# Kernel tuning notes

Hardware: AMD Instinct MI355X
Metric: run time of the kernel (lower is better)

## Reference

```python
import jax, jax.numpy as jnp
import numpy as np

N = 10000
E = 160000
F_IN = 2000
HID = 128
NC = 5


def setup_inputs() -> dict:
    key = jax.random.key(0)
    ks = jax.random.split(key, 16)
    s = 0.05
    nrm = lambda k, shape: jax.random.normal(k, shape, jnp.float32) * s
    return {
        "x": jax.random.normal(ks[0], (N, F_IN), jnp.float32),
        "edge_index": jax.random.randint(ks[1], (2, E), 0, N),
        # GATConv 1: in=F_IN, out=HID, heads=6, concat=False
        "W_gat1": nrm(ks[2], (F_IN, 6 * HID)), "a_src1": nrm(ks[3], (6, HID)),
        "a_dst1": nrm(ks[4], (6, HID)), "b_gat1": jnp.zeros(HID, jnp.float32),
        # GCNConv 1
        "W_gcn1": nrm(ks[5], (HID, HID)), "b_gcn1": jnp.zeros(HID, jnp.float32),
        # GATConv 2: heads=4
        "W_gat2": nrm(ks[6], (HID, 4 * HID)), "a_src2": nrm(ks[7], (4, HID)),
        "a_dst2": nrm(ks[8], (4, HID)), "b_gat2": jnp.zeros(HID, jnp.float32),
        # GCNConv 2: out=HID//2
        "W_gcn2": nrm(ks[9], (HID, HID // 2)), "b_gcn2": jnp.zeros(HID // 2, jnp.float32),
        # skip projection / fusion
        "W_skip": nrm(ks[10], (F_IN, HID // 2)), "b_skip": jnp.zeros(HID // 2, jnp.float32),
        "W_fuse": nrm(ks[11], (HID + HID // 2, HID // 2)), "b_fuse": jnp.zeros(HID // 2, jnp.float32),
        # classifier MLP
        "W_c1": nrm(ks[12], (HID // 2, HID // 4)), "b_c1": jnp.zeros(HID // 4, jnp.float32),
        "W_c2": nrm(ks[13], (HID // 4, HID // 8)), "b_c2": jnp.zeros(HID // 8, jnp.float32),
        "W_c3": nrm(ks[14], (HID // 8, NC)), "b_c3": jnp.zeros(NC, jnp.float32),
        # LayerNorms
        "g1": jnp.ones(HID, jnp.float32), "be1": jnp.zeros(HID, jnp.float32),
        "g2": jnp.ones(HID, jnp.float32), "be2": jnp.zeros(HID, jnp.float32),
        "g3": jnp.ones(HID // 2, jnp.float32), "be3": jnp.zeros(HID // 2, jnp.float32),
    }


def layer_norm(x, g, b, eps=1e-5):
    mu = jnp.mean(x, axis=-1, keepdims=True)
    var = jnp.var(x, axis=-1, keepdims=True)
    return (x - mu) * jax.lax.rsqrt(var + eps) * g + b


def gat_conv(x, src, dst, W, a_src, a_dst, b, n):
    # PyG GATConv with concat=False (head-mean). Eval mode -> no attn dropout.
    H, C = a_src.shape
    h = (x @ W).reshape(-1, H, C)                      # [N,H,C]
    alpha = (h * a_src).sum(-1)[src] + (h * a_dst).sum(-1)[dst]  # [E,H]
    alpha = jax.nn.leaky_relu(alpha, 0.2)
    m = jax.ops.segment_max(alpha, dst, num_segments=n)
    e = jnp.exp(alpha - m[dst])
    w = e / jax.ops.segment_sum(e, dst, num_segments=n)[dst]     # segment softmax over incoming edges
    out = jax.ops.segment_sum(h[src] * w[:, :, None], dst, num_segments=n)  # [N,H,C]
    return out.mean(axis=1) + b


def gcn_conv(x, src, dst, W, b, n):
    deg = jax.ops.segment_sum(jnp.ones_like(dst, x.dtype), dst, num_segments=n)
    dinv = jnp.where(deg > 0, deg ** -0.5, 0.0)
    msg = (x @ W)[src] * (dinv[src] * dinv[dst])[:, None]
    return jax.ops.segment_sum(msg, dst, num_segments=n) + b


def reference(x, edge_index, W_gat1, a_src1, a_dst1, b_gat1, W_gcn1, b_gcn1,
              W_gat2, a_src2, a_dst2, b_gat2, W_gcn2, b_gcn2,
              W_skip, b_skip, W_fuse, b_fuse, W_c1, b_c1, W_c2, b_c2, W_c3, b_c3,
              g1, be1, g2, be2, g3, be3):
    n = x.shape[0]
    loop = jnp.arange(n, dtype=edge_index.dtype)
    src = jnp.concatenate([edge_index[0], loop])  # add_self_loops
    dst = jnp.concatenate([edge_index[1], loop])

    x1_gat = jax.nn.relu(layer_norm(gat_conv(x, src, dst, W_gat1, a_src1, a_dst1, b_gat1, n), g1, be1))
    x1_gcn = jax.nn.relu(gcn_conv(x1_gat, src, dst, W_gcn1, b_gcn1, n))
    x2_gat = jax.nn.relu(layer_norm(gat_conv(x1_gcn, src, dst, W_gat2, a_src2, a_dst2, b_gat2, n), g2, be2))
    x2_gcn = jax.nn.relu(gcn_conv(x2_gat, src, dst, W_gcn2, b_gcn2, n))

    skip = jax.nn.relu(x @ W_skip + b_skip)
    fused = jax.nn.relu(jnp.concatenate([x1_gcn, x2_gcn], axis=1) @ W_fuse + b_fuse)
    final = layer_norm(fused + skip, g3, be3)

    h = jax.nn.relu(final @ W_c1 + b_c1)
    h = jax.nn.relu(h @ W_c2 + b_c2)
    return h @ W_c3 + b_c3
```

## Files before the change

### kernel.cpp

```cpp
#include <hip/hip_runtime.h>
#include <cstdint>
#include <cstddef>

#define NN 10000
#define NE 160000
#define ET (NE + NN)
#define FIN 2000
#define MPAD 10112
#define KPAD 2048
#define NPAD 896

typedef __bf16 bf16x8 __attribute__((ext_vector_type(8)));
typedef __bf16 bf16x4 __attribute__((ext_vector_type(4)));
typedef float  f32x4  __attribute__((ext_vector_type(4)));

#define GLL(src, dst) __builtin_amdgcn_global_load_lds( \
    (const __attribute__((address_space(1))) void*)(src), \
    (__attribute__((address_space(3))) void*)(dst), 16, 0, 0)

__device__ __forceinline__ void edge_sd(const int* ei, int e, int& s, int& d) {
    if (e < NE) { s = ei[e]; d = ei[NE + e]; }
    else        { s = e - NE; d = e - NE; }
}

__global__ void scan_kernel(const int* deg, int* rowstart, float* dinv) {
    __shared__ int partial[256];
    const int T = 256;
    int chunk = (NN + T - 1) / T;
    int t = threadIdx.x;
    int begin = t * chunk;
    int end = begin + chunk; if (end > NN) end = NN;
    int s = 0;
    for (int i = begin; i < end && i >= begin; i++) s += deg[i];
    partial[t] = s;
    __syncthreads();
    if (t == 0) {
        int run = 0;
        for (int i = 0; i < T; i++) { int v = partial[i]; partial[i] = run; run += v; }
    }
    __syncthreads();
    int run = partial[t];
    for (int i = begin; i < end && i >= begin; i++) {
        rowstart[i] = run; run += deg[i];
        int dg = deg[i];
        dinv[i] = dg > 0 ? rsqrtf((float)dg) : 0.f;
    }
    if (end == NN && begin <= NN) rowstart[NN] = run;
}

__global__ void scatter_kernel(const int* ei, const int* rowstart, int* cursor,
                               int* csr_src) {
    int e = blockIdx.x * blockDim.x + threadIdx.x;
    if (e >= ET) return;
    int s, d; edge_sd(ei, e, s, d);
    int pos = atomicAdd(&cursor[d], 1);
    csr_src[rowstart[d] + pos] = s;
}

#define NBX (158 * 8)
#define NW1 (NPAD * KPAD / 8)
#define NWT (NW1 + 512 * 128 / 8)
#define NWT2 (NWT + 2048 + 1024)
#define WBLK ((NWT2 + 255) / 256)
#define EB 665
__global__ void conv_kernel(const float* __restrict__ x, __bf16* __restrict__ xb,
                            const float* __restrict__ Wg, const float* __restrict__ Ws,
                            const float* __restrict__ W2,
                            const float* __restrict__ Wg1, const float* __restrict__ Wg2,
                            __bf16* __restrict__ wt, __bf16* __restrict__ w2t,
                            __bf16* __restrict__ wgcn1s, __bf16* __restrict__ wgcn2s,
                            const int* __restrict__ ei, int* __restrict__ deg) {
    __shared__ __bf16 ls[16384];
    int bid = blockIdx.x;
    int tid = threadIdx.x;
    if (bid < NBX) {
        int rt = bid >> 3, kb = bid & 7;
        const int lane16 = tid & 15;
        const int ksl = lane16 >> 2;
        const int p0 = (lane16 & 3) * 2;
        const int rbase = tid >> 4;
        const int kg0 = kb * 256 + lane16 * 16;
        const int rsw_x = (p0 & 6) ^ ksl;
#pragma unroll
        for (int pass = 0; pass < 4; pass++) {
            int r = pass * 16 + rbase;
            int row = rt * 64 + r;
            bf16x8 v0, v1;
#pragma unroll
            for (int j = 0; j < 4; j++) {
                int k = kg0 + j * 4;
                f32x4 f;
                if (row < NN && k + 3 < FIN)
                    f = *(const f32x4*)(x + (size_t)row * FIN + k);
                else
                    f = (f32x4){0.f, 0.f, 0.f, 0.f};
                int o = (j & 1) * 4;
                if (j < 2) {
                    v0[o] = (__bf16)f[0]; v0[o+1] = (__bf16)f[1];
                    v0[o+2] = (__bf16)f[2]; v0[o+3] = (__bf16)f[3];
                } else {
                    v1[o] = (__bf16)f[0]; v1[o+1] = (__bf16)f[1];
                    v1[o+2] = (__bf16)f[2]; v1[o+3] = (__bf16)f[3];
                }
            }
            int rsw = r ^ rsw_x;
            *(bf16x8*)(ls + (((ksl * 8 + p0) * 64 + rsw) * 8))     = v0;
            *(bf16x8*)(ls + (((ksl * 8 + p0 + 1) * 64 + rsw) * 8)) = v1;
        }
        __syncthreads();
        size_t cbase = ((size_t)rt * 32 + kb * 4) * 512;
#pragma unroll
        for (int i = 0; i < 8; i++) {
            int g = i * 256 + tid;
            int ksl2 = g >> 9, rem = g & 511;
            int p = rem >> 6, rr = rem & 63;
            int rsw = rr ^ ((p & 6) ^ ksl2);
            bf16x8 v = *(const bf16x8*)(ls + (((ksl2 * 8 + p) * 64 + rsw) * 8));
            *(bf16x8*)(xb + (cbase + (size_t)ksl2 * 512 + (p * 64 + rr)) * 8) = v;
        }
    } else if (bid < NBX + WBLK) {
        int g = (bid - NBX) * 256 + tid;
        if (g < NW1) {
            int r = g & 127, p = (g >> 7) & 7, ks = (g >> 10) & 31, ct = g >> 15;
            int n = ct * 128 + r;
            int k0 = ks * 64 + p * 8;
            bf16x8 o;
#pragma unroll
            for (int j = 0; j < 8; j++) {
                int k = k0 + j;
                float v = 0.f;
                if (k < FIN) {
                    if (n < 768)      v = Wg[(size_t)k * 768 + n];
                    else if (n < 832) v = Ws[(size_t)k * 64 + (n - 768)];
                }
                o[j] = (__bf16)v;
            }
            *(bf16x8*)(wt + (size_t)g * 8) = o;
        } else if (g < NWT) {
            int g2 = g - NW1;
            int c = g2 & 2047;
            int ct = g2 >> 11;
            int p = c >> 7, r = c & 127;
            int n = ct * 128 + r;
            int k0 = p * 8;
            bf16x8 o;
#pragma unroll
            for (int j = 0; j < 8; j++)
                o[j] = (__bf16)W2[(size_t)(k0 + j) * 512 + n];
            *(bf16x8*)(w2t + (size_t)g2 * 8) = o;
        } else if (g < NWT + 2048) {
            int g3 = g - NWT;
            int p = g3 >> 7, r = g3 & 127;
            bf16x8 o;
#pragma unroll
            for (int j = 0; j < 8; j++)
                o[j] = (__bf16)Wg1[(size_t)(p * 8 + j) * 128 + r];
            *(bf16x8*)(wgcn1s + (size_t)g3 * 8) = o;
        } else if (g < NWT2) {
            int g4 = g - NWT - 2048;
            int p = g4 >> 6, r = g4 & 63;
            bf16x8 o;
#pragma unroll
            for (int j = 0; j < 8; j++)
                o[j] = (__bf16)Wg2[(size_t)(p * 8 + j) * 64 + r];
            *(bf16x8*)(wgcn2s + (size_t)g4 * 8) = o;
        }
    } else {
        int e = (bid - NBX - WBLK) * 256 + tid;
        if (e < ET) {
            int s, d; edge_sd(ei, e, s, d);
            atomicAdd(&deg[d], 1);
        }
    }
}

__global__ __launch_bounds__(512)
void mfma_gemm1_kernel(const __bf16* __restrict__ xb, const __bf16* __restrict__ wt,
                       const float* __restrict__ a_src1, const float* __restrict__ a_dst1,
                       __bf16* __restrict__ h1b, float* __restrict__ skippre,
                       float* __restrict__ asrc, float* __restrict__ adst) {
    __shared__ __bf16 As[8192];
    __shared__ __bf16 Bs[8192];
    __shared__ float sA[128], sD[128];
    __shared__ float asd[256];
    int b = blockIdx.x;
    int xcd = b & 7, j = b >> 3;
    int jq = j / 7;
    int rt = xcd + 8 * jq;
    int ct = j - 7 * jq;
    if (rt >= MPAD / 128) return;
    const int bi = rt * 128;
    const int bn = ct * 128;

    const int tid = threadIdx.x;
    const int lane = tid & 63;
    const int w = tid >> 6;
    const int wm = w >> 1;
    const int wn = w & 1;
    const int q = lane >> 4, m16 = lane & 15;

    if (tid < 128) { sA[tid] = 0.f; sD[tid] = 0.f; }
    if (ct < 6) {
        if (tid < 128)      asd[tid] = a_src1[ct * 128 + tid];
        else if (tid < 256) asd[tid] = a_dst1[ct * 128 + (tid - 128)];
    }

    f32x4 acc[2][4] = {};

    for (int ks = 0; ks < KPAD / 64; ks++) {
        const size_t slabA = ((size_t)(rt * 2) * 32 + ks) * 512;
        const size_t slabB = ((size_t)ct * 32 + ks) * 1024;
#pragma unroll
        for (int i = 0; i < 2; i++) {
            int seg = i * 8 + w;
            int p = seg >> 1, h = seg & 1;
            GLL(xb + (slabA + (size_t)h * 16384 + p * 64 + lane) * 8,
                As + seg * 512);
        }
#pragma unroll
        for (int i = 0; i < 2; i++) {
            int seg = i * 8 + w;
            GLL(wt + (slabB + seg * 64 + lane) * 8, Bs + seg * 512);
        }
        __syncthreads();

#pragma unroll
        for (int kk = 0; kk < 2; kk++) {
            const int pb = kk * 4 + q;
            bf16x8 af[2], bfr[4];
#pragma unroll
            for (int mt = 0; mt < 2; mt++)
                af[mt] = *(const bf16x8*)(As + (pb * 128 + wm * 32 + mt * 16 + m16) * 8);
#pragma unroll
            for (int nt = 0; nt < 4; nt++)
                bfr[nt] = *(const bf16x8*)(Bs + (pb * 128 + wn * 64 + nt * 16 + m16) * 8);
#pragma unroll
            for (int mt = 0; mt < 2; mt++)
#pragma unroll
                for (int nt = 0; nt < 4; nt++)
                    acc[mt][nt] = __builtin_amdgcn_mfma_f32_16x16x32_bf16(af[mt], bfr[nt], acc[mt][nt], 0, 0, 0);
        }
        __syncthreads();
    }

#pragma unroll
    for (int mt = 0; mt < 2; mt++) {
#pragma unroll
        for (int r = 0; r < 4; r++) {
            int rowl = wm * 32 + mt * 16 + q * 4 + r;
            int row = bi + rowl;
            float ps = 0.f, pd = 0.f;
#pragma unroll
            for (int nt = 0; nt < 4; nt++) {
                int coll = wn * 64 + nt * 16 + m16;
                int col = bn + coll;
                float v = acc[mt][nt][r];
                if (ct < 6) { ps += v * asd[coll]; pd += v * asd[128 + coll]; }
                if (row < NN) {
                    if (col < 768)      h1b[(size_t)row * 768 + col] = (__bf16)v;
                    else if (col < 832) skippre[(size_t)row * 64 + (col - 768)] = v;
                }
            }
            if (ct < 6) {
#pragma unroll
                for (int off = 1; off < 16; off <<= 1) {
                    ps += __shfl_xor(ps, off);
                    pd += __shfl_xor(pd, off);
                }
                if (m16 == 0) { atomicAdd(&sA[rowl], ps); atomicAdd(&sD[rowl], pd); }
            }
        }
    }
    if (ct < 6) {
        __syncthreads();
        if (tid < 128) {
            int row = bi + tid;
            if (row < NN) { asrc[row * 6 + ct] = sA[tid]; adst[row * 6 + ct] = sD[tid]; }
        }
    }
}

__global__ __launch_bounds__(256)
void mfma_gemm2_kernel(const __bf16* __restrict__ A, const __bf16* __restrict__ B,
                       const float* __restrict__ a_src2, const float* __restrict__ a_dst2,
                       __bf16* __restrict__ h2b,
                       float* __restrict__ asrc, float* __restrict__ adst) {
    __shared__ __bf16 As[4096];
    __shared__ __bf16 Bs[8192];
    __shared__ float sA[64], sD[64];
    __shared__ float asd[256];
    const int rt = blockIdx.y, ct = blockIdx.x;
    const int bi = rt * 64, bn = ct * 128;
    const int tid = threadIdx.x, lane = tid & 63, w = tid >> 6;
    const int wm = w >> 1, wn = w & 1;
    const int q = lane >> 4, m16 = lane & 15;

    if (tid < 64) { sA[tid] = 0.f; sD[tid] = 0.f; }
    if (tid < 128) asd[tid] = a_src2[ct * 128 + tid];
    else           asd[tid] = a_dst2[ct * 128 + (tid - 128)];

    f32x4 acc[2][4] = {};

    for (int ks = 0; ks < 2; ks++) {
        const size_t slabA = (size_t)rt * 1024 + ks * 512;
        const size_t slabB = (size_t)ct * 2048 + ks * 1024;
#pragma unroll
        for (int i = 0; i < 2; i++) {
            int seg = i * 4 + w;
            GLL(A + (slabA + seg * 64 + lane) * 8, As + seg * 512);
        }
#pragma unroll
        for (int i = 0; i < 4; i++) {
            int seg = i * 4 + w;
            GLL(B + (slabB + seg * 64 + lane) * 8, Bs + seg * 512);
        }
        __syncthreads();

#pragma unroll
        for (int kk = 0; kk < 2; kk++) {
            const int pb = kk * 4 + q;
            bf16x8 af[2], bfr[4];
#pragma unroll
            for (int mt = 0; mt < 2; mt++)
                af[mt] = *(const bf16x8*)(As + (pb * 64 + wm * 32 + mt * 16 + m16) * 8);
#pragma unroll
            for (int nt = 0; nt < 4; nt++)
                bfr[nt] = *(const bf16x8*)(Bs + (pb * 128 + wn * 64 + nt * 16 + m16) * 8);
#pragma unroll
            for (int mt = 0; mt < 2; mt++)
#pragma unroll
                for (int nt = 0; nt < 4; nt++)
                    acc[mt][nt] = __builtin_amdgcn_mfma_f32_16x16x32_bf16(af[mt], bfr[nt], acc[mt][nt], 0, 0, 0);
        }
        __syncthreads();
    }

#pragma unroll
    for (int mt = 0; mt < 2; mt++) {
#pragma unroll
        for (int r = 0; r < 4; r++) {
            int rowl = wm * 32 + mt * 16 + q * 4 + r;
            int row = bi + rowl;
            float ps = 0.f, pd = 0.f;
#pragma unroll
            for (int nt = 0; nt < 4; nt++) {
                int coll = wn * 64 + nt * 16 + m16;
                float v = acc[mt][nt][r];
                ps += v * asd[coll]; pd += v * asd[128 + coll];
                if (row < NN) h2b[(size_t)row * 512 + bn + coll] = (__bf16)v;
            }
#pragma unroll
            for (int off = 1; off < 16; off <<= 1) {
                ps += __shfl_xor(ps, off);
                pd += __shfl_xor(pd, off);
            }
            if (m16 == 0) { atomicAdd(&sA[rowl], ps); atomicAdd(&sD[rowl], pd); }
        }
    }
    __syncthreads();
    if (tid < 64) {
        int row = bi + tid;
        if (row < NN) { asrc[row * 4 + ct] = sA[tid]; adst[row * 4 + ct] = sD[tid]; }
    }
}

template<int NT>
__global__ __launch_bounds__(256)
void mfma_gcn_kernel(const __bf16* __restrict__ A, const __bf16* __restrict__ B,
                     __bf16* __restrict__ Cb) {
    __shared__ __bf16 As[4096];
    __shared__ __bf16 Bs[NT * 64];
    const int rt = blockIdx.x;
    const int bi = rt * 64;
    const int tid = threadIdx.x, lane = tid & 63, w = tid >> 6;
    const int q = lane >> 4, m16 = lane & 15;
    constexpr int MT = (NT == 128) ? 2 : 1;
    constexpr int MSPAN = (NT == 128) ? 32 : 16;
    const int wm = (NT == 128) ? (w >> 1) : w;
    const int wn = (NT == 128) ? (w & 1) : 0;

    f32x4 acc[MT][4] = {};

    for (int ks = 0; ks < 2; ks++) {
        const size_t slabA = (size_t)rt * 1024 + ks * 512;
        const size_t slabB = (size_t)ks * (NT * 8);
#pragma unroll
        for (int i = 0; i < 2; i++) {
            int seg = i * 4 + w;
            GLL(A + (slabA + seg * 64 + lane) * 8, As + seg * 512);
        }
#pragma unroll
        for (int i = 0; i < NT / 32; i++) {
            int seg = i * 4 + w;
            GLL(B + (slabB + (size_t)seg * 64 + lane) * 8, Bs + seg * 512);
        }
        __syncthreads();

#pragma unroll
        for (int kk = 0; kk < 2; kk++) {
            const int pb = kk * 4 + q;
            bf16x8 af[MT], bfr[4];
#pragma unroll
            for (int mt = 0; mt < MT; mt++)
                af[mt] = *(const bf16x8*)(As + (pb * 64 + wm * MSPAN + mt * 16 + m16) * 8);
#pragma unroll
            for (int nt = 0; nt < 4; nt++)
                bfr[nt] = *(const bf16x8*)(Bs + (pb * NT + wn * 64 + nt * 16 + m16) * 8);
#pragma unroll
            for (int mt = 0; mt < MT; mt++)
#pragma unroll
                for (int nt = 0; nt < 4; nt++)
                    acc[mt][nt] = __builtin_amdgcn_mfma_f32_16x16x32_bf16(af[mt], bfr[nt], acc[mt][nt], 0, 0, 0);
        }
        __syncthreads();
    }

#pragma unroll
    for (int mt = 0; mt < MT; mt++) {
#pragma unroll
        for (int r = 0; r < 4; r++) {
            int row = bi + wm * MSPAN + mt * 16 + q * 4 + r;
            if (row >= NN) continue;
#pragma unroll
            for (int nt = 0; nt < 4; nt++) {
                int col = wn * 64 + nt * 16 + m16;
                Cb[(size_t)row * NT + col] = (__bf16)acc[mt][nt][r];
            }
        }
    }
}

template<int H>
__global__ void gat_agg_kernel(const __bf16* __restrict__ hb,
                               const float* __restrict__ asrc,
                               const float* __restrict__ adst,
                               const int* __restrict__ rowstart,
                               const int* __restrict__ csr_src,
                               const float* __restrict__ bias,
                               const float* __restrict__ gamma,
                               const float* __restrict__ beta,
                               __bf16* __restrict__ outs) {
    constexpr int CH = H * 128;
    constexpr int CAP = 128;
    int n = blockIdx.x;
    int t = threadIdx.x;
    int w = t >> 6, l = t & 63;
    __shared__ float invden[H];
    __shared__ float denp[256];
    __shared__ int   srcs[CAP];
    __shared__ float evs[CAP * H];
    __shared__ float sm[4 * CH];
    __shared__ float red[8];

    int s0 = rowstart[n];
    int deg = rowstart[n + 1] - s0;
    float adst_n = (l < H) ? adst[n * H + l] : 0.f;

    const int eh = t >> 3;
    const int hh1 = t & 7;
    float adst_h = (hh1 < H) ? adst[n * H + hh1] : 0.f;
    float dloc = 0.f;
    for (int base = 0; base < deg; base += 32) {
        int idx = base + eh;
        if (idx < deg) {
            int src = csr_src[s0 + idx];
            if (hh1 == 0 && idx < CAP) srcs[idx] = src;
            if (hh1 < H) {
                float al = asrc[src * H + hh1] + adst_h;
                al = al >= 0.f ? al : 0.2f * al;
                float ev = __expf(al);
                dloc += ev;
                if (idx < CAP) evs[idx * H + hh1] = ev;
            }
        }
    }
    denp[t] = dloc;
    __syncthreads();
    if (t < H) {
        float s = 0.f;
#pragma unroll
        for (int g = 0; g < 32; g++) s += denp[g * 8 + t];
        invden[t] = 1.f / s;
    }
    __syncthreads();

    constexpr int NA = (H == 6) ? 12 : 8;
    float acc[NA] = {};
    const int h0 = l >> 4;
    const int h1i = 4 + (l >> 5);
    int degc = deg < CAP ? deg : CAP;
    int idx = w;
    for (; idx + 4 < degc; idx += 8) {
        int src0 = srcs[idx], src1 = srcs[idx + 4];
        float w00 = evs[idx * H + h0];
        float w10 = evs[(idx + 4) * H + h0];
        const __bf16* hp0 = hb + (size_t)src0 * CH;
        const __bf16* hp1 = hb + (size_t)src1 * CH;
        bf16x8 g00 = *(const bf16x8*)(hp0 + l * 8);
        bf16x8 g10 = *(const bf16x8*)(hp1 + l * 8);
#pragma unroll
        for (int jj = 0; jj < 8; jj++)
            acc[jj] += (float)g00[jj] * w00 + (float)g10[jj] * w10;
        if (H == 6) {
            float w01 = evs[idx * H + h1i];
            float w11 = evs[(idx + 4) * H + h1i];
            bf16x4 g01 = *(const bf16x4*)(hp0 + 512 + l * 4);
            bf16x4 g11 = *(const bf16x4*)(hp1 + 512 + l * 4);
#pragma unroll
            for (int jj = 0; jj < 4; jj++)
                acc[8 + jj] += (float)g01[jj] * w01 + (float)g11[jj] * w11;
        }
    }
    if (idx < degc) {
        int src = srcs[idx];
        float w0 = evs[idx * H + h0];
        const __bf16* hp = hb + (size_t)src * CH;
        bf16x8 hv = *(const bf16x8*)(hp + l * 8);
#pragma unroll
        for (int jj = 0; jj < 8; jj++) acc[jj] += (float)hv[jj] * w0;
        if (H == 6) {
            float w1 = evs[idx * H + h1i];
            bf16x4 hv1 = *(const bf16x4*)(hp + 512 + l * 4);
#pragma unroll
            for (int jj = 0; jj < 4; jj++) acc[8 + jj] += (float)hv1[jj] * w1;
        }
    }
    for (int i2 = CAP + w; i2 < deg; i2 += 4) {
        int src = csr_src[s0 + i2];
        float ev = 0.f;
        if (l < H) {
            float al = asrc[src * H + l] + adst_n;
            al = al >= 0.f ? al : 0.2f * al;
            ev = __expf(al);
        }
        const __bf16* hp = hb + (size_t)src * CH;
        float wgt = __shfl(ev, h0);
        bf16x8 hv = *(const bf16x8*)(hp + l * 8);
#pragma unroll
        for (int jj = 0; jj < 8; jj++) acc[jj] += (float)hv[jj] * wgt;
        if (H == 6) {
            float wg1 = __shfl(ev, h1i);
            bf16x4 hv1 = *(const bf16x4*)(hp + 512 + l * 4);
#pragma unroll
            for (int jj = 0; jj < 4; jj++) acc[8 + jj] += (float)hv1[jj] * wg1;
        }
    }

    *(f32x4*)(sm + w * CH + l * 8)     = *(f32x4*)(acc);
    *(f32x4*)(sm + w * CH + l * 8 + 4) = *(f32x4*)(acc + 4);
    if (H == 6)
        *(f32x4*)(sm + w * CH + 512 + l * 4) = *(f32x4*)(acc + 8);
    __syncthreads();

    float v = 0.f;
    if (t < 128) {
#pragma unroll
        for (int hh = 0; hh < H; hh++) {
            float hsum = 0.f;
#pragma unroll
            for (int ww = 0; ww < 4; ww++) hsum += sm[ww * CH + hh * 128 + t];
            v += hsum * invden[hh];
        }
        v = v * (1.f / H) + bias[t];
    }
    float sv = (t < 128) ? v : 0.f;
    float sq = (t < 128) ? v * v : 0.f;
#pragma unroll
    for (int off = 32; off; off >>= 1) {
        sv += __shfl_down(sv, off);
        sq += __shfl_down(sq, off);
    }
    if ((t & 63) == 0) { red[w * 2] = sv; red[w * 2 + 1] = sq; }
    __syncthreads();
    float tot = red[0] + red[2] + red[4] + red[6];
    float tsq = red[1] + red[3] + red[5] + red[7];
    float mu = tot * (1.f / 128.f);
    float var = tsq * (1.f / 128.f) - mu * mu;
    float r = rsqrtf(var + 1e-5f);
    if (t < 128) {
        float o = fmaxf((v - mu) * r * gamma[t] + beta[t], 0.f);
        int rt2 = n >> 6, rr = n & 63, pp = t >> 3, off2 = t & 7;
        outs[((size_t)(rt2 * 16 + pp) * 64 + rr) * 8 + off2] = (__bf16)o;
    }
}

__global__ void gcn_agg_kernel(const __bf16* __restrict__ y, int C,
                               const float* __restrict__ dinv,
                               const int* __restrict__ rowstart,
                               const int* __restrict__ csr_src,
                               const float* __restrict__ bias,
                               float* __restrict__ out, int ldo, int coloff,
                               __bf16* __restrict__ bout) {
    int n = blockIdx.x;
    int t = threadIdx.x;
    float acc = 0.f;
    int s0 = rowstart[n], s1 = rowstart[n + 1];
    for (int s = s0; s < s1; s++) {
        int src = csr_src[s];
        acc += (float)y[(size_t)src * C + t] * dinv[src];
    }
    float v = fmaxf(acc * dinv[n] + bias[t], 0.f);
    out[(size_t)n * ldo + coloff + t] = v;
    if (bout) {
        int rt = n >> 6, r = n & 63, p = t >> 3, off = t & 7;
        bout[((size_t)(rt * 16 + p) * 64 + r) * 8 + off] = (__bf16)v;
    }
}

__global__ __launch_bounds__(256)
void fuse_final_kernel(const float* __restrict__ cat,
                       const float* __restrict__ skippre,
                       const float* __restrict__ Wf, const float* __restrict__ bfz,
                       const float* __restrict__ b_skip,
                       const float* __restrict__ g3, const float* __restrict__ be3,
                       const float* __restrict__ Wc1, const float* __restrict__ bc1,
                       const float* __restrict__ Wc2, const float* __restrict__ bc2,
                       const float* __restrict__ Wc3, const float* __restrict__ bc3,
                       float* __restrict__ out) {
    __shared__ float WfS[192 * 64];
    __shared__ float catS[4][196];
    __shared__ float fS[4][64], h1S[4][32], h2S[4][16];
    int tid = threadIdx.x;
    int w = tid >> 6, l = tid & 63;
#pragma unroll
    for (int i = 0; i < 12; i++) {
        int idx = (i * 256 + tid) * 4;
        *(f32x4*)(WfS + idx) = *(const f32x4*)(Wf + idx);
    }
    int n = blockIdx.x * 4 + w;
    bool act = n < NN;
    float sk = 0.f;
    if (act) {
        catS[w][l]       = cat[(size_t)n * 192 + l];
        catS[w][64 + l]  = cat[(size_t)n * 192 + 64 + l];
        catS[w][128 + l] = cat[(size_t)n * 192 + 128 + l];
        sk = fmaxf(skippre[(size_t)n * 64 + l] + b_skip[l], 0.f);
    }
    __syncthreads();

    float fu = bfz[l];
#pragma unroll 4
    for (int k = 0; k < 192; k++)
        fu += catS[w][k] * WfS[k * 64 + l];
    float v = fmaxf(fu, 0.f) + sk;

    float sv = v, sq = v * v;
#pragma unroll
    for (int off = 32; off; off >>= 1) {
        sv += __shfl_xor(sv, off);
        sq += __shfl_xor(sq, off);
    }
    float mu = sv * (1.f / 64.f);
    float var = sq * (1.f / 64.f) - mu * mu;
    float r = rsqrtf(var + 1e-5f);
    fS[w][l] = (v - mu) * r * g3[l] + be3[l];
    __syncthreads();
    if (l < 32) {
        float a = bc1[l];
        for (int i = 0; i < 64; i++) a += fS[w][i] * Wc1[i * 32 + l];
        h1S[w][l] = fmaxf(a, 0.f);
    }
    __syncthreads();
    if (l < 16) {
        float a = bc2[l];
        for (int i = 0; i < 32; i++) a += h1S[w][i] * Wc2[i * 16 + l];
        h2S[w][l] = fmaxf(a, 0.f);
    }
    __syncthreads();
    if (l < 5 && act) {
        float a = bc3[l];
        for (int i = 0; i < 16; i++) a += h2S[w][i] * Wc3[i * 5 + l];
        out[(size_t)n * 5 + l] = a;
    }
}

extern "C" void kernel_launch(void* const* d_in, const int* in_sizes, int n_in,
                              void* d_out, int out_size, void* d_ws, size_t ws_size,
                              hipStream_t stream) {
    const float* x      = (const float*)d_in[0];
    const int*   ei     = (const int*)d_in[1];
    const float* W_gat1 = (const float*)d_in[2];
    const float* a_src1 = (const float*)d_in[3];
    const float* a_dst1 = (const float*)d_in[4];
    const float* b_gat1 = (const float*)d_in[5];
    const float* W_gcn1 = (const float*)d_in[6];
    const float* b_gcn1 = (const float*)d_in[7];
    const float* W_gat2 = (const float*)d_in[8];
    const float* a_src2 = (const float*)d_in[9];
    const float* a_dst2 = (const float*)d_in[10];
    const float* b_gat2 = (const float*)d_in[11];
    const float* W_gcn2 = (const float*)d_in[12];
    const float* b_gcn2 = (const float*)d_in[13];
    const float* W_skip = (const float*)d_in[14];
    const float* b_skip = (const float*)d_in[15];
    const float* W_fuse = (const float*)d_in[16];
    const float* b_fuse = (const float*)d_in[17];
    const float* W_c1   = (const float*)d_in[18];
    const float* b_c1   = (const float*)d_in[19];
    const float* W_c2   = (const float*)d_in[20];
    const float* b_c2   = (const float*)d_in[21];
    const float* W_c3   = (const float*)d_in[22];
    const float* b_c3   = (const float*)d_in[23];
    const float* g1     = (const float*)d_in[24];
    const float* be1    = (const float*)d_in[25];
    const float* g2     = (const float*)d_in[26];
    const float* be2    = (const float*)d_in[27];
    const float* g3     = (const float*)d_in[28];
    const float* be3    = (const float*)d_in[29];
    float* out = (float*)d_out;

    char* p = (char*)d_ws;
    auto alloc = [&](size_t bytes) {
        char* r = p; p += (bytes + 255) & ~(size_t)255; return r;
    };
    __bf16* xb      = (__bf16*)alloc((size_t)MPAD * KPAD * 2);
    __bf16* wt      = (__bf16*)alloc((size_t)NPAD * KPAD * 2);
    __bf16* w2t     = (__bf16*)alloc((size_t)512 * 128 * 2);
    __bf16* wgcn1s  = (__bf16*)alloc((size_t)128 * 128 * 2);
    __bf16* wgcn2s  = (__bf16*)alloc((size_t)64 * 128 * 2);
    __bf16* h1b     = (__bf16*)alloc((size_t)NN * 768 * 2);
    __bf16* h2b     = (__bf16*)alloc((size_t)NN * 512 * 2);
    __bf16* ybufb   = (__bf16*)alloc((size_t)NN * 128 * 2);
    __bf16* x1gatb  = (__bf16*)alloc((size_t)3 * MPAD * 128 * 2);
    __bf16* x1gcnb  = x1gatb + (size_t)MPAD * 128;
    __bf16* x2gatb  = x1gcnb + (size_t)MPAD * 128;
    float* asrc     = (float*)alloc((size_t)NN * 6 * 4);
    float* adst     = (float*)alloc((size_t)NN * 6 * 4);
    int*   deg      = (int*)  alloc((size_t)2 * NN * 4);
    int*   cursor   = deg + NN;
    float* dinv     = (float*)alloc((size_t)NN * 4);
    int*   rowst    = (int*)  alloc((size_t)(NN + 1) * 4);
    int*   csrc     = (int*)  alloc((size_t)ET * 4);
    float* cat      = (float*)alloc((size_t)NN * 192 * 4);
    float* skippre  = (float*)alloc((size_t)NN * 64 * 4);

    hipMemsetAsync(deg, 0, (size_t)2 * NN * 4, stream);
    hipMemsetAsync(x1gatb, 0, (size_t)3 * MPAD * 128 * 2, stream);

    conv_kernel<<<NBX + WBLK + EB, 256, 0, stream>>>(
        x, xb, W_gat1, W_skip, W_gat2, W_gcn1, W_gcn2,
        wt, w2t, wgcn1s, wgcn2s, ei, deg);

    scan_kernel   <<<1, 256, 0, stream>>>(deg, rowst, dinv);
    scatter_kernel<<<EB, 256, 0, stream>>>(ei, rowst, cursor, csrc);

    mfma_gemm1_kernel<<<560, 512, 0, stream>>>(xb, wt, a_src1, a_dst1,
                                               h1b, skippre, asrc, adst);

    gat_agg_kernel<6><<<NN, 256, 0, stream>>>(h1b, asrc, adst, rowst, csrc,
                                              b_gat1, g1, be1, x1gatb);
    mfma_gcn_kernel<128><<<MPAD / 64, 256, 0, stream>>>(x1gatb, wgcn1s, ybufb);
    gcn_agg_kernel<<<NN, 128, 0, stream>>>(ybufb, 128, dinv, rowst, csrc,
                                           b_gcn1, cat, 192, 0, x1gcnb);
    mfma_gemm2_kernel<<<dim3(4, MPAD / 64), 256, 0, stream>>>(
        x1gcnb, w2t, a_src2, a_dst2, h2b, asrc, adst);
    gat_agg_kernel<4><<<NN, 256, 0, stream>>>(h2b, asrc, adst, rowst, csrc,
                                              b_gat2, g2, be2, x2gatb);
    mfma_gcn_kernel<64><<<MPAD / 64, 256, 0, stream>>>(x2gatb, wgcn2s, ybufb);
    gcn_agg_kernel<<<NN, 64, 0, stream>>>(ybufb, 64, dinv, rowst, csrc,
                                          b_gcn2, cat, 192, 128, nullptr);
    fuse_final_kernel<<<(NN + 3) / 4, 256, 0, stream>>>(
        cat, skippre, W_fuse, b_fuse, b_skip, g3, be3,
        W_c1, b_c1, W_c2, b_c2, W_c3, b_c3, out);
}
```

Before: 430.1 us.

## Parallelize scan, vectorize GCN aggregation, batch nodes per wave in fuse kernel

The single-block scan replaces its serial thread-0 prefix with wave shuffle scans plus a small cross-wave sum. GCN aggregation now splits each node's edges across groups of lanes that load 8 bf16 values at once, then reduces the partial sums through shared memory. The fuse/classifier kernel processes 4 nodes per wave, so the W_fuse shared-memory load is amortized over 16 nodes per block instead of 4. The fused kernel drops its __syncthreads between layers and relies on intra-wave ordering of the shared-memory fS/h1S/h2S buffers, which is a correctness risk if the wave does not execute in lockstep.

```diff
diff --git a/kernel.cpp b/kernel.cpp
--- a/kernel.cpp
+++ b/kernel.cpp
@@ -24,28 +24,32 @@
 }
 
 __global__ void scan_kernel(const int* deg, int* rowstart, float* dinv) {
-    __shared__ int partial[256];
+    __shared__ int wsum[4];
     const int T = 256;
     int chunk = (NN + T - 1) / T;
     int t = threadIdx.x;
     int begin = t * chunk;
     int end = begin + chunk; if (end > NN) end = NN;
+    if (begin > NN) begin = NN;
     int s = 0;
-    for (int i = begin; i < end && i >= begin; i++) s += deg[i];
-    partial[t] = s;
+    for (int i = begin; i < end; i++) s += deg[i];
+    int inc = s;
+#pragma unroll
+    for (int off = 1; off < 64; off <<= 1) {
+        int u = __shfl_up(inc, off);
+        if ((t & 63) >= off) inc += u;
+    }
+    if ((t & 63) == 63) wsum[t >> 6] = inc;
     __syncthreads();
-    if (t == 0) {
-        int run = 0;
-        for (int i = 0; i < T; i++) { int v = partial[i]; partial[i] = run; run += v; }
-    }
-    __syncthreads();
-    int run = partial[t];
-    for (int i = begin; i < end && i >= begin; i++) {
+    int woff = 0;
+    for (int wv = 0; wv < (t >> 6); wv++) woff += wsum[wv];
+    int run = woff + inc - s;
+    for (int i = begin; i < end; i++) {
         rowstart[i] = run; run += deg[i];
         int dg = deg[i];
         dinv[i] = dg > 0 ? rsqrtf((float)dg) : 0.f;
     }
-    if (end == NN && begin <= NN) rowstart[NN] = run;
+    if (end == NN) rowstart[NN] = run;
 }
 
 __global__ void scatter_kernel(const int* ei, const int* rowstart, int* cursor,
@@ -584,26 +588,43 @@
     }
 }
 
-__global__ void gcn_agg_kernel(const __bf16* __restrict__ y, int C,
+template<int C>
+__global__ void gcn_agg_kernel(const __bf16* __restrict__ y,
                                const float* __restrict__ dinv,
                                const int* __restrict__ rowstart,
                                const int* __restrict__ csr_src,
                                const float* __restrict__ bias,
-                               float* __restrict__ out, int ldo, int coloff,
+                               float* __restrict__ out, int coloff,
                                __bf16* __restrict__ bout) {
+    constexpr int LPE = C / 8;
+    constexpr int G = 128 / LPE;
+    __shared__ float sm[G * C];
     int n = blockIdx.x;
     int t = threadIdx.x;
-    float acc = 0.f;
+    int lane = t & (LPE - 1);
+    int grp = t / LPE;
+    float acc[8] = {};
     int s0 = rowstart[n], s1 = rowstart[n + 1];
-    for (int s = s0; s < s1; s++) {
-        int src = csr_src[s];
-        acc += (float)y[(size_t)src * C + t] * dinv[src];
-    }
-    float v = fmaxf(acc * dinv[n] + bias[t], 0.f);
-    out[(size_t)n * ldo + coloff + t] = v;
-    if (bout) {
-        int rt = n >> 6, r = n & 63, p = t >> 3, off = t & 7;
-        bout[((size_t)(rt * 16 + p) * 64 + r) * 8 + off] = (__bf16)v;
+    for (int e = s0 + grp; e < s1; e += G) {
+        int src = csr_src[e];
+        float dv = dinv[src];
+        bf16x8 v = *(const bf16x8*)(y + (size_t)src * C + lane * 8);
+#pragma unroll
+        for (int j = 0; j < 8; j++) acc[j] += (float)v[j] * dv;
+    }
+    *(f32x4*)(sm + grp * C + lane * 8)     = *(f32x4*)(acc);
+    *(f32x4*)(sm + grp * C + lane * 8 + 4) = *(f32x4*)(acc + 4);
+    __syncthreads();
+    if (t < C) {
+        float v = 0.f;
+#pragma unroll
+        for (int g = 0; g < G; g++) v += sm[g * C + t];
+        v = fmaxf(v * dinv[n] + bias[t], 0.f);
+        out[(size_t)n * 192 + coloff + t] = v;
+        if (bout) {
+            int rt = n >> 6, r = n & 63, p = t >> 3, off = t & 7;
+            bout[((size_t)(rt * 16 + p) * 64 + r) * 8 + off] = (__bf16)v;
+        }
     }
 }
 
@@ -618,7 +639,7 @@
                        const float* __restrict__ Wc3, const float* __restrict__ bc3,
                        float* __restrict__ out) {
     __shared__ float WfS[192 * 64];
-    __shared__ float catS[4][196];
+    __shared__ float catS[4][4][196];
     __shared__ float fS[4][64], h1S[4][32], h2S[4][16];
     int tid = threadIdx.x;
     int w = tid >> 6, l = tid & 63;
@@ -627,50 +648,58 @@
         int idx = (i * 256 + tid) * 4;
         *(f32x4*)(WfS + idx) = *(const f32x4*)(Wf + idx);
     }
-    int n = blockIdx.x * 4 + w;
-    bool act = n < NN;
-    float sk = 0.f;
-    if (act) {
-        catS[w][l]       = cat[(size_t)n * 192 + l];
-        catS[w][64 + l]  = cat[(size_t)n * 192 + 64 + l];
-        catS[w][128 + l] = cat[(size_t)n * 192 + 128 + l];
-        sk = fmaxf(skippre[(size_t)n * 64 + l] + b_skip[l], 0.f);
+    int n0 = blockIdx.x * 16 + w * 4;
+    float sk[4];
+#pragma unroll
+    for (int i = 0; i < 4; i++) {
+        int n = n0 + i;
+        if (n < NN) {
+            catS[w][i][l]       = cat[(size_t)n * 192 + l];
+            catS[w][i][64 + l]  = cat[(size_t)n * 192 + 64 + l];
+            catS[w][i][128 + l] = cat[(size_t)n * 192 + 128 + l];
+            sk[i] = fmaxf(skippre[(size_t)n * 64 + l] + b_skip[l], 0.f);
+        } else {
+            sk[i] = 0.f;
+        }
     }
     __syncthreads();
 
-    float fu = bfz[l];
+#pragma unroll
+    for (int i = 0; i < 4; i++) {
+        int n = n0 + i;
+        if (n < NN) {
+            float fu = bfz[l];
 #pragma unroll 4
-    for (int k = 0; k < 192; k++)
-        fu += catS[w][k] * WfS[k * 64 + l];
-    float v = fmaxf(fu, 0.f) + sk;
-
-    float sv = v, sq = v * v;
-#pragma unroll
-    for (int off = 32; off; off >>= 1) {
-        sv += __shfl_xor(sv, off);
-        sq += __shfl_xor(sq, off);
-    }
-    float mu = sv * (1.f / 64.f);
-    float var = sq * (1.f / 64.f) - mu * mu;
-    float r = rsqrtf(var + 1e-5f);
-    fS[w][l] = (v - mu) * r * g3[l] + be3[l];
-    __syncthreads();
-    if (l < 32) {
-        float a = bc1[l];
-        for (int i = 0; i < 64; i++) a += fS[w][i] * Wc1[i * 32 + l];
-        h1S[w][l] = fmaxf(a, 0.f);
-    }
-    __syncthreads();
-    if (l < 16) {
-        float a = bc2[l];
-        for (int i = 0; i < 32; i++) a += h1S[w][i] * Wc2[i * 16 + l];
-        h2S[w][l] = fmaxf(a, 0.f);
-    }
-    __syncthreads();
-    if (l < 5 && act) {
-        float a = bc3[l];
-        for (int i = 0; i < 16; i++) a += h2S[w][i] * Wc3[i * 5 + l];
-        out[(size_t)n * 5 + l] = a;
+            for (int k = 0; k < 192; k++)
+                fu += catS[w][i][k] * WfS[k * 64 + l];
+            float v = fmaxf(fu, 0.f) + sk[i];
+
+            float sv = v, sq = v * v;
+#pragma unroll
+            for (int off = 32; off; off >>= 1) {
+                sv += __shfl_xor(sv, off);
+                sq += __shfl_xor(sq, off);
+            }
+            float mu = sv * (1.f / 64.f);
+            float var = sq * (1.f / 64.f) - mu * mu;
+            float r = rsqrtf(var + 1e-5f);
+            fS[w][l] = (v - mu) * r * g3[l] + be3[l];
+            if (l < 32) {
+                float a = bc1[l];
+                for (int k = 0; k < 64; k++) a += fS[w][k] * Wc1[k * 32 + l];
+                h1S[w][l] = fmaxf(a, 0.f);
+            }
+            if (l < 16) {
+                float a = bc2[l];
+                for (int k = 0; k < 32; k++) a += h1S[w][k] * Wc2[k * 16 + l];
+                h2S[w][l] = fmaxf(a, 0.f);
+            }
+            if (l < 5) {
+                float a = bc3[l];
+                for (int k = 0; k < 16; k++) a += h2S[w][k] * Wc3[k * 5 + l];
+                out[(size_t)n * 5 + l] = a;
+            }
+        }
     }
 }
 
@@ -750,16 +779,16 @@
     gat_agg_kernel<6><<<NN, 256, 0, stream>>>(h1b, asrc, adst, rowst, csrc,
                                               b_gat1, g1, be1, x1gatb);
     mfma_gcn_kernel<128><<<MPAD / 64, 256, 0, stream>>>(x1gatb, wgcn1s, ybufb);
-    gcn_agg_kernel<<<NN, 128, 0, stream>>>(ybufb, 128, dinv, rowst, csrc,
-                                           b_gcn1, cat, 192, 0, x1gcnb);
+    gcn_agg_kernel<128><<<NN, 128, 0, stream>>>(ybufb, dinv, rowst, csrc,
+                                                b_gcn1, cat, 0, x1gcnb);
     mfma_gemm2_kernel<<<dim3(4, MPAD / 64), 256, 0, stream>>>(
         x1gcnb, w2t, a_src2, a_dst2, h2b, asrc, adst);
     gat_agg_kernel<4><<<NN, 256, 0, stream>>>(h2b, asrc, adst, rowst, csrc,
                                               b_gat2, g2, be2, x2gatb);
     mfma_gcn_kernel<64><<<MPAD / 64, 256, 0, stream>>>(x2gatb, wgcn2s, ybufb);
-    gcn_agg_kernel<<<NN, 64, 0, stream>>>(ybufb, 64, dinv, rowst, csrc,
-                                          b_gcn2, cat, 192, 128, nullptr);
-    fuse_final_kernel<<<(NN + 3) / 4, 256, 0, stream>>>(
+    gcn_agg_kernel<64><<<NN, 128, 0, stream>>>(ybufb, dinv, rowst, csrc,
+                                               b_gcn2, cat, 128, nullptr);
+    fuse_final_kernel<<<(NN + 15) / 16, 256, 0, stream>>>(
         cat, skippre, W_fuse, b_fuse, b_skip, g3, be3,
         W_c1, b_c1, W_c2, b_c2, W_c3, b_c3, out);
 }
```

Measured after the change: 417.4 us. 1.03x faster.
